# Kernel optimization log

Hardware: AMD Instinct MI355X
Metric: run time of the kernel (lower is better)

The kernel has to match this reference:

```python
import jax, jax.numpy as jnp
import numpy as np

H = 2048
MAX_DEPTH = 2
BASIS = 4


def setup_inputs() -> dict:
    key = jax.random.key(0)
    ks = jax.random.split(key, 16)
    s = 0.02

    def w(k, shape):
        return jax.random.normal(k, shape, dtype=jnp.float32) * s

    return dict(
        x=jax.random.normal(ks[0], (1, H), dtype=jnp.float32),
        h=jax.random.normal(ks[1], (1, H), dtype=jnp.float32),
        c=jax.random.normal(ks[2], (1, H), dtype=jnp.float32),
        Wq=w(ks[3], (H, H)), Wk=w(ks[4], (H, H)), Wv=w(ks[5], (H, H)), Wo=w(ks[6], (H, H)),
        Wih=w(ks[7], (H, 4 * H)), Whh=w(ks[8], (H, 4 * H)),
        b_lstm=jnp.zeros((4 * H,), jnp.float32),
        router_w=w(ks[9], (H, BASIS)), router_b=jnp.zeros((BASIS,), jnp.float32),
        expert_w=w(ks[10], (BASIS, H, H)), expert_b=jnp.zeros((BASIS, H), jnp.float32),
        dr_w=w(ks[11], (H, MAX_DEPTH + 1)),
        # bias the depth router toward the deepest choice so the recursion tree is exercised
        dr_b=jnp.array([0.0, 1.0, 5.0], jnp.float32),
        ram_w=w(ks[12], (2 * H, H)), ram_b=jnp.zeros((H,), jnp.float32),
        ag_w=w(ks[13], (2 * H, H)), ag_b=jnp.zeros((H,), jnp.float32),
    )


def reference(x, h, c, Wq, Wk, Wv, Wo, Wih, Whh, b_lstm, router_w, router_b,
              expert_w, expert_b, dr_w, dr_b, ram_w, ram_b, ag_w, ag_b):
    def cell_step(x_, h_, c_):
        # Single-token multi-head attention: softmax over a length-1 axis is
        # identically 1, so attention collapses to (h @ Wv) @ Wo; Wq/Wk are
        # parameters with zero effective gradient (matches torch behavior).
        attn = (h_ @ Wv) @ Wo
        gates = x_ @ Wih + attn @ Whh + b_lstm  # [1, 4H]
        i, f, g, o = jnp.split(gates, 4, axis=1)
        c2 = jax.nn.sigmoid(f) * c_ + jax.nn.sigmoid(i) * jnp.tanh(g)
        h2 = jax.nn.sigmoid(o) * jnp.tanh(c2)
        return h2, h2, c2

    def path_gate(hh):
        p = jax.nn.softmax(hh @ router_w + router_b, axis=1)          # [1, E]
        eo = jnp.einsum('bh,ehk->bek', hh, expert_w) + expert_b        # [1, E, H]
        return jnp.einsum('be,bek->bk', p, eo)                         # [1, H]

    def ramanujan(states):
        # alternating-harmonic (Ramanujan-summation style) weighted reduction
        agg = states[0] * 0.0
        for n, s in enumerate(states):
            agg = agg + (((-1.0) ** n) / (n + 1)) * s
        return jnp.concatenate([agg, states[0]], axis=1) @ ram_w + ram_b

    def fwd(x_, h_, c_, depth):
        so, hs, cs = cell_step(x_, h_, c_)
        hp = path_gate(hs)
        # mirrors torch.no_grad() + .item() host sync
        chosen = int(jnp.argmax(hp @ dr_w + dr_b, axis=1)[0])
        steps = min(chosen, max(0, MAX_DEPTH - depth))
        if steps <= 0:
            return so, hp, cs
        h_cur, c_cur, final = hp, cs, so
        states = [h_cur]
        for _ in range(steps):
            damping = 1.0 / (depth + 1) ** 2
            ro, hnr, cn = fwd(x_, h_cur, c_cur, depth + 1)
            h_next = h_cur + damping * (hnr - h_cur)  # torch.lerp
            states.append(h_next)
            h_cur, c_cur, final = h_next, cn, ro
        anchor = ramanujan(states)
        g = jax.nn.sigmoid(jnp.concatenate([h_cur, anchor], axis=1) @ ag_w + ag_b)
        return final, g * anchor + (1.0 - g) * h_cur, c_cur

    return fwd(x, h, c, 0)
```

## Files before the change

### kernel.cpp

```cpp
#include <hip/hip_runtime.h>
#include <math.h>


#define H 2048

#define DL0 0
#define DL1 4
#define DL3 8
#define GT  16
#define NODE_BASE (16 + 8192)
#define NODESZ 26624
#define O_THV   0
#define O_ATTN  2048
#define O_GATES 4096
#define O_EO    12288
#define O_SO    20480
#define O_CS    22528
#define O_HP    24576
#define FIN_BASE (NODE_BASE + 5 * NODESZ)
#define FINSZ 8192
#define O_HN     0
#define O_AGG    2048
#define O_ANCHOR 4096
#define O_GACC   6144
#define RH1 (FIN_BASE + 3 * FINSZ)
#define RF1 (RH1 + 2048)
#define RC1 (RH1 + 4096)

__device__ __forceinline__ float sigm(float v) { return 1.f / (1.f + expf(-v)); }

__device__ __forceinline__ int dsteps(const float* dl, int maxSteps) {
  float l0 = dl[0], l1 = dl[1], l2 = dl[2];
  int ch = 0; float bv = l0;
  if (l1 > bv) { bv = l1; ch = 1; }
  if (l2 > bv) { bv = l2; ch = 2; }
  return ch < maxSteps ? ch : maxSteps;
}

__device__ __forceinline__ bool pred_ok(const float* dlA, int maxA, int needA,
                                        const float* dlB, int maxB, int needB) {
  if (dlA && dsteps(dlA, maxA) < needA) return false;
  if (dlB && dsteps(dlB, maxB) < needB) return false;
  return true;
}

__global__ void k_init(float* ws, const float* b_lstm, const float* expert_b,
                       const float* ram_b, const float* ag_b, const float* dr_b) {
  const int gtid = blockIdx.x * 256 + threadIdx.x;
  const int gsz = gridDim.x * 256;
  if (gtid < 3) { ws[DL0 + gtid] = dr_b[gtid]; ws[DL1 + gtid] = dr_b[gtid]; ws[DL3 + gtid] = dr_b[gtid]; }
  for (int i = gtid; i < 8192; i += gsz) ws[GT + i] = b_lstm[i];
  for (int n = 0; n < 5; ++n) {
    float* nb = ws + NODE_BASE + n * NODESZ;
    for (int i = gtid; i < 4096; i += gsz) nb[O_THV + i] = 0.f;
    for (int i = gtid; i < 8192; i += gsz) nb[O_EO + i] = expert_b[i];
  }
  for (int f = 0; f < 3; ++f) {
    float* fb = ws + FIN_BASE + f * FINSZ;
    for (int i = gtid; i < 2048; i += gsz) { fb[O_ANCHOR + i] = ram_b[i]; fb[O_GACC + i] = ag_b[i]; }
  }
}

__global__ void k_gemv(const float* __restrict__ xA, const float* __restrict__ xB, int splitPt,
                       const float* __restrict__ W, float* __restrict__ y,
                       int K, int N, int KS,
                       const float* dlA, int maxA, int needA,
                       const float* dlB, int maxB, int needB,
                       const float* copySrc, float* copyDst, int copyN)
{
  if (!pred_ok(dlA, maxA, needA, dlB, maxB, needB)) return;
  const int tid = threadIdx.x, lane = tid & 63, tsub = tid >> 6;
  if (copySrc) {
    int gid = blockIdx.x * 256 + tid;
    if (gid < copyN) copyDst[gid] = copySrc[gid];
  }
  const int G = N >> 8;
  const int g = blockIdx.x % G;
  const int s = blockIdx.x / G;
  const int chunk = K / KS, len = chunk >> 2;
  const int i0 = s * chunk + tsub * len;
  const int j = (g << 8) + (lane << 2);
  const float* Wp = W + (size_t)i0 * N + j;
  float ax = 0.f, ay = 0.f, az = 0.f, aw = 0.f;
  for (int t = 0; t < len; ++t) {
    const int i = i0 + t;
    const float xi = (i < splitPt) ? xA[i] : xB[i - splitPt];
    const float4 wv = *reinterpret_cast<const float4*>(Wp);
    ax = fmaf(xi, wv.x, ax); ay = fmaf(xi, wv.y, ay);
    az = fmaf(xi, wv.z, az); aw = fmaf(xi, wv.w, aw);
    Wp += N;
  }
  __shared__ float4 red[256];
  red[tid] = make_float4(ax, ay, az, aw);
  __syncthreads();
  if (tsub == 0) {
    float4 a = red[tid], b = red[tid + 64], c = red[tid + 128], d = red[tid + 192];
    atomicAdd(&y[j + 0], a.x + b.x + c.x + d.x);
    atomicAdd(&y[j + 1], a.y + b.y + c.y + d.y);
    atomicAdd(&y[j + 2], a.z + b.z + c.z + d.z);
    atomicAdd(&y[j + 3], a.w + b.w + c.w + d.w);
  }
}

__global__ void k_expert(const float* __restrict__ gates, const float* __restrict__ c_in,
                         const float* __restrict__ Wex, float* __restrict__ eo,
                         float* so, float* cs,
                         const float* dlA, int maxA, int needA,
                         const float* dlB, int maxB, int needB)
{
  if (!pred_ok(dlA, maxA, needA, dlB, maxB, needB)) return;
  const int tid = threadIdx.x, lane = tid & 63, w = tid >> 6;
  const int g = blockIdx.x & 31, s = blockIdx.x >> 5;
  const int i0 = s * 128;
  __shared__ float h2s[128];
  if (tid < 128) {
    const int i = i0 + tid;
    const float gi = gates[i], gf = gates[H + i], gg = gates[2 * H + i], go = gates[3 * H + i];
    const float c2 = sigm(gf) * c_in[i] + sigm(gi) * tanhf(gg);
    const float h2 = sigm(go) * tanhf(c2);
    h2s[tid] = h2;
    if (g == 0) { so[i] = h2; cs[i] = c2; }
  }
  __syncthreads();
  const int j = (g << 8) + (lane << 2);
  const int e = j >> 11, k = j & (H - 1);
  const float* Wp = Wex + ((size_t)e << 22) + (size_t)(i0 + w * 32) * H + k;
  float ax = 0.f, ay = 0.f, az = 0.f, aw = 0.f;
  for (int t = 0; t < 32; ++t) {
    const float xi = h2s[w * 32 + t];
    const float4 wv = *reinterpret_cast<const float4*>(Wp);
    ax = fmaf(xi, wv.x, ax); ay = fmaf(xi, wv.y, ay);
    az = fmaf(xi, wv.z, az); aw = fmaf(xi, wv.w, aw);
    Wp += H;
  }
  __shared__ float4 red[256];
  red[tid] = make_float4(ax, ay, az, aw);
  __syncthreads();
  if (w == 0) {
    float4 a = red[tid], b = red[tid + 64], c = red[tid + 128], d = red[tid + 192];
    atomicAdd(&eo[j + 0], a.x + b.x + c.x + d.x);
    atomicAdd(&eo[j + 1], a.y + b.y + c.y + d.y);
    atomicAdd(&eo[j + 2], a.z + b.z + c.z + d.z);
    atomicAdd(&eo[j + 3], a.w + b.w + c.w + d.w);
  }
}

template <int LEAF>
__global__ void k_combine(const float* __restrict__ h2,
                          const float* __restrict__ router_w, const float* __restrict__ router_b,
                          const float* __restrict__ eo,
                          float* hp_out, float* dl, const float* __restrict__ dr_w,
                          const float* php, float damping, float* hn_out, float* agg_out,
                          const float* dlA, int maxA, int needA,
                          const float* dlB, int maxB, int needB)
{
  if (!pred_ok(dlA, maxA, needA, dlB, maxB, needB)) return;
  const int tid = threadIdx.x;
  float r0 = 0.f, r1 = 0.f, r2 = 0.f, r3 = 0.f;
  for (int i = tid; i < H; i += 256) {
    const float hh = h2[i];
    const float4 rw = *reinterpret_cast<const float4*>(router_w + i * 4);
    r0 = fmaf(hh, rw.x, r0); r1 = fmaf(hh, rw.y, r1);
    r2 = fmaf(hh, rw.z, r2); r3 = fmaf(hh, rw.w, r3);
  }
  __shared__ float4 red[256];
  red[tid] = make_float4(r0, r1, r2, r3);
  __syncthreads();
  for (int off = 128; off > 0; off >>= 1) {
    if (tid < off) {
      float4 b = red[tid + off];
      red[tid].x += b.x; red[tid].y += b.y; red[tid].z += b.z; red[tid].w += b.w;
    }
    __syncthreads();
  }
  const float4 L = red[0];
  __syncthreads();
  const float l0 = L.x + router_b[0], l1 = L.y + router_b[1];
  const float l2 = L.z + router_b[2], l3 = L.w + router_b[3];
  const float m = fmaxf(fmaxf(l0, l1), fmaxf(l2, l3));
  const float e0 = expf(l0 - m), e1 = expf(l1 - m), e2 = expf(l2 - m), e3 = expf(l3 - m);
  const float inv = 1.f / (e0 + e1 + e2 + e3);
  const float p0 = e0 * inv, p1 = e1 * inv, p2 = e2 * inv, p3 = e3 * inv;
  const int jj = blockIdx.x * 256 + tid;
  const float v = p0 * eo[jj] + p1 * eo[H + jj] + p2 * eo[2 * H + jj] + p3 * eo[3 * H + jj];
  if (LEAF) {
    const float h0 = php[jj];
    const float hn = h0 + damping * (v - h0);
    hn_out[jj] = hn;
    agg_out[jj] = h0 - 0.5f * hn;
  } else {
    hp_out[jj] = v;
    const float d0 = v * dr_w[jj * 3 + 0];
    const float d1 = v * dr_w[jj * 3 + 1];
    const float d2 = v * dr_w[jj * 3 + 2];
    red[tid] = make_float4(d0, d1, d2, 0.f);
    __syncthreads();
    for (int off = 128; off > 0; off >>= 1) {
      if (tid < off) {
        float4 b = red[tid + off];
        red[tid].x += b.x; red[tid].y += b.y; red[tid].z += b.z;
      }
      __syncthreads();
    }
    if (tid == 0) {
      atomicAdd(&dl[0], red[0].x);
      atomicAdd(&dl[1], red[0].y);
      atomicAdd(&dl[2], red[0].z);
    }
  }
}

__global__ void k_fsel(const float* dlC, int maxC,
                       const float* gacc, const float* anchor, const float* hn,
                       const float* soL, const float* csL,
                       const float* hpN, const float* soN, const float* csN,
                       float* rh, float* rf, float* rc,
                       const float* dlA, int maxA, int needA)
{
  if (dlA && dsteps(dlA, maxA) < needA) return;
  const int jj = blockIdx.x * 256 + threadIdx.x;
  if (dsteps(dlC, maxC) >= 1) {
    const float gv = sigm(gacc[jj]);
    rh[jj] = gv * anchor[jj] + (1.f - gv) * hn[jj];
    rf[jj] = soL[jj]; rc[jj] = csL[jj];
  } else {
    rh[jj] = hpN[jj]; rf[jj] = soN[jj]; rc[jj] = csN[jj];
  }
}

__global__ void k_tail1(const float* dl0p, const float* dl3p,
                        const float* rh1, const float* rf1, const float* rc1,
                        const float* gacc3, const float* anchor3, const float* hn3,
                        const float* so4, const float* cs4,
                        const float* hp3, const float* so3, const float* cs3,
                        const float* hp0,
                        float* agg0, float* hcur0, float* outF, float* outC)
{
  const int s0v = dsteps(dl0p, 2);
  if (s0v < 1) return;
  const int jj = blockIdx.x * 256 + threadIdx.x;
  float rh3 = 0.f, rf3 = 0.f, rc3 = 0.f;
  if (s0v >= 2) {
    if (dsteps(dl3p, 1) >= 1) {
      const float gv = sigm(gacc3[jj]);
      rh3 = gv * anchor3[jj] + (1.f - gv) * hn3[jj];
      rf3 = so4[jj]; rc3 = cs4[jj];
    } else { rh3 = hp3[jj]; rf3 = so3[jj]; rc3 = cs3[jj]; }
  }
  const float r1 = rh1[jj];
  float ag = hp0[jj] - 0.5f * r1;
  float hc, oF, oC;
  if (s0v >= 2) { ag += (1.f / 3.f) * rh3; hc = rh3; oF = rf3; oC = rc3; }
  else { hc = r1; oF = rf1[jj]; oC = rc1[jj]; }
  agg0[jj] = ag; hcur0[jj] = hc; outF[jj] = oF; outC[jj] = oC;
}

__global__ void k_tail2(const float* dl0p,
                        const float* so0, const float* hp0, const float* cs0,
                        const float* gacc0, const float* anchor0, const float* hcur0,
                        float* out)
{
  const int s0v = dsteps(dl0p, 2);
  const int jj = blockIdx.x * 256 + threadIdx.x;
  if (s0v == 0) {
    out[jj] = so0[jj]; out[H + jj] = hp0[jj]; out[2 * H + jj] = cs0[jj];
  } else {
    const float gv = sigm(gacc0[jj]);
    out[H + jj] = gv * anchor0[jj] + (1.f - gv) * hcur0[jj];
  }
}

extern "C" void kernel_launch(void* const* d_in, const int* in_sizes, int n_in,
                              void* d_out, int out_size, void* d_ws, size_t ws_size,
                              hipStream_t stream) {
  const float* x        = (const float*)d_in[0];
  const float* h0in     = (const float*)d_in[1];
  const float* c0in     = (const float*)d_in[2];
  const float* Wv       = (const float*)d_in[5];
  const float* Wo       = (const float*)d_in[6];
  const float* Wih      = (const float*)d_in[7];
  const float* Whh      = (const float*)d_in[8];
  const float* b_lstm   = (const float*)d_in[9];
  const float* router_w = (const float*)d_in[10];
  const float* router_b = (const float*)d_in[11];
  const float* expert_w = (const float*)d_in[12];
  const float* expert_b = (const float*)d_in[13];
  const float* dr_w     = (const float*)d_in[14];
  const float* dr_b     = (const float*)d_in[15];
  const float* ram_w    = (const float*)d_in[16];
  const float* ram_b    = (const float*)d_in[17];
  const float* ag_w     = (const float*)d_in[18];
  const float* ag_b     = (const float*)d_in[19];
  float* out = (float*)d_out;
  float* ws  = (float*)d_ws;

  float* dl0 = ws + DL0; float* dl1 = ws + DL1; float* dl3 = ws + DL3;
  float* gt  = ws + GT;
  auto NB = [&](int n) { return ws + NODE_BASE + n * NODESZ; };
  float* fin1 = ws + FIN_BASE;
  float* fin3 = ws + FIN_BASE + FINSZ;
  float* fin0 = ws + FIN_BASE + 2 * FINSZ;
  float* rh1 = ws + RH1; float* rf1 = ws + RF1; float* rc1 = ws + RC1;

  auto gemv = [&](const float* xA, const float* xB, int splitPt,
                  const float* W, float* y, int K, int N, int KS,
                  const float* dlA, int maxA, int needA,
                  const float* dlB, int maxB, int needB,
                  const float* cpS, float* cpD, int cpN) {
    k_gemv<<<dim3((N >> 8) * KS), dim3(256), 0, stream>>>(
        xA, xB, splitPt, W, y, K, N, KS, dlA, maxA, needA, dlB, maxB, needB, cpS, cpD, cpN);
  };

  auto node = [&](int n, const float* hv, const float* cv,
                  float* dl, float damping, const float* php, float* hn_out, float* agg_out,
                  const float* dlA, int maxA, int needA,
                  const float* dlB, int maxB, int needB) {
    float* nb = NB(n);
    float* t_hv = nb + O_THV; float* attn = nb + O_ATTN; float* gates = nb + O_GATES;
    float* eo = nb + O_EO; float* so = nb + O_SO; float* cs = nb + O_CS; float* hp = nb + O_HP;
    gemv(hv, hv, H, Wv, t_hv, H, H, 64, dlA, maxA, needA, dlB, maxB, needB, gt, gates, 4 * H);
    gemv(t_hv, t_hv, H, Wo, attn, H, H, 64, dlA, maxA, needA, dlB, maxB, needB, nullptr, nullptr, 0);
    gemv(attn, attn, H, Whh, gates, H, 4 * H, 16, dlA, maxA, needA, dlB, maxB, needB, nullptr, nullptr, 0);
    k_expert<<<dim3(512), dim3(256), 0, stream>>>(gates, cv, expert_w, eo, so, cs,
                                                  dlA, maxA, needA, dlB, maxB, needB);
    if (dl) {
      k_combine<0><<<dim3(8), dim3(256), 0, stream>>>(so, router_w, router_b, eo, hp, dl, dr_w,
                                                      nullptr, 0.f, nullptr, nullptr,
                                                      dlA, maxA, needA, dlB, maxB, needB);
    } else {
      k_combine<1><<<dim3(8), dim3(256), 0, stream>>>(so, router_w, router_b, eo, nullptr, nullptr, nullptr,
                                                      php, damping, hn_out, agg_out,
                                                      dlA, maxA, needA, dlB, maxB, needB);
    }
  };

  k_init<<<dim3(192), dim3(256), 0, stream>>>(ws, b_lstm, expert_b, ram_b, ag_b, dr_b);
  gemv(x, x, H, Wih, gt, H, 4 * H, 16, nullptr, 0, 0, nullptr, 0, 0, nullptr, nullptr, 0);

  node(0, h0in, c0in, dl0, 0.f, nullptr, nullptr, nullptr,
       nullptr, 0, 0, nullptr, 0, 0);
  node(1, NB(0) + O_HP, NB(0) + O_CS, dl1, 0.f, nullptr, nullptr, nullptr,
       dl0, 2, 1, nullptr, 0, 0);
  node(2, NB(1) + O_HP, NB(1) + O_CS, nullptr, 0.25f, NB(1) + O_HP, fin1 + O_HN, fin1 + O_AGG,
       dl0, 2, 1, dl1, 1, 1);
  gemv(fin1 + O_AGG, NB(1) + O_HP, H, ram_w, fin1 + O_ANCHOR, 2 * H, H, 64,
       dl0, 2, 1, dl1, 1, 1, nullptr, nullptr, 0);
  gemv(fin1 + O_HN, fin1 + O_ANCHOR, H, ag_w, fin1 + O_GACC, 2 * H, H, 64,
       dl0, 2, 1, dl1, 1, 1, nullptr, nullptr, 0);
  k_fsel<<<dim3(8), dim3(256), 0, stream>>>(dl1, 1,
      fin1 + O_GACC, fin1 + O_ANCHOR, fin1 + O_HN,
      NB(2) + O_SO, NB(2) + O_CS,
      NB(1) + O_HP, NB(1) + O_SO, NB(1) + O_CS,
      rh1, rf1, rc1, dl0, 2, 1);

  node(3, rh1, rc1, dl3, 0.f, nullptr, nullptr, nullptr,
       dl0, 2, 2, nullptr, 0, 0);
  node(4, NB(3) + O_HP, NB(3) + O_CS, nullptr, 0.25f, NB(3) + O_HP, fin3 + O_HN, fin3 + O_AGG,
       dl0, 2, 2, dl3, 1, 1);
  gemv(fin3 + O_AGG, NB(3) + O_HP, H, ram_w, fin3 + O_ANCHOR, 2 * H, H, 64,
       dl0, 2, 2, dl3, 1, 1, nullptr, nullptr, 0);
  gemv(fin3 + O_HN, fin3 + O_ANCHOR, H, ag_w, fin3 + O_GACC, 2 * H, H, 64,
       dl0, 2, 2, dl3, 1, 1, nullptr, nullptr, 0);

  k_tail1<<<dim3(8), dim3(256), 0, stream>>>(dl0, dl3,
      rh1, rf1, rc1,
      fin3 + O_GACC, fin3 + O_ANCHOR, fin3 + O_HN,
      NB(4) + O_SO, NB(4) + O_CS,
      NB(3) + O_HP, NB(3) + O_SO, NB(3) + O_CS,
      NB(0) + O_HP,
      fin0 + O_AGG, fin0 + O_HN, out, out + 2 * H);
  gemv(fin0 + O_AGG, NB(0) + O_HP, H, ram_w, fin0 + O_ANCHOR, 2 * H, H, 64,
       dl0, 2, 1, nullptr, 0, 0, nullptr, nullptr, 0);
  gemv(fin0 + O_HN, fin0 + O_ANCHOR, H, ag_w, fin0 + O_GACC, 2 * H, H, 64,
       dl0, 2, 1, nullptr, 0, 0, nullptr, nullptr, 0);
  k_tail2<<<dim3(8), dim3(256), 0, stream>>>(dl0,
      NB(0) + O_SO, NB(0) + O_HP, NB(0) + O_CS,
      fin0 + O_GACC, fin0 + O_ANCHOR, fin0 + O_HN, out);
}
```

Measured before the change: 406.2 us.

## Convert recurrent weights to bf16 per call and fuse combine/tail kernels via last-block counters

Each call now converts Wv, Wo, Whh and the expert weights to bf16 in a workspace region, and the per-node GEMVs and expert kernel stream those bf16 weights with 8-wide loads. Halving the bytes read over the five node passes is meant to cut the HBM traffic that dominates these GEMVs, even after paying the conversion traffic once per call. The router/combine step and the fsel/tail steps are folded into the preceding kernels using an atomic last-block counter, and fixed 256-block grids replace the per-shape launch sizes. This reduces launch count, but it costs bf16 rounding error in the recurrence and adds threadfence/atomic serialization at the end of each kernel.

```diff
diff --git a/kernel.cpp b/kernel.cpp
--- a/kernel.cpp
+++ b/kernel.cpp
@@ -3,116 +3,250 @@
 
 
 #define H 2048
-
-#define DL0 0
-#define DL1 4
-#define DL3 8
-#define GT  16
-#define NODE_BASE (16 + 8192)
-#define NODESZ 26624
-#define O_THV   0
-#define O_ATTN  2048
-#define O_GATES 4096
-#define O_EO    12288
-#define O_SO    20480
-#define O_CS    22528
-#define O_HP    24576
-#define FIN_BASE (NODE_BASE + 5 * NODESZ)
-#define FINSZ 8192
-#define O_HN     0
-#define O_AGG    2048
-#define O_ANCHOR 4096
-#define O_GACC   6144
-#define RH1 (FIN_BASE + 3 * FINSZ)
-#define RF1 (RH1 + 2048)
-#define RC1 (RH1 + 4096)
+typedef unsigned short u16;
+
+constexpr int DL_OFF   = 16;
+constexpr int GT_OFF   = 32;
+constexpr int NODE_OFF = 8224;
+constexpr int NODESZ   = 26624;
+constexpr int THVo = 0, ATTNo = 2048, GATESo = 4096, EOo = 12288, SOo = 20480, CSo = 22528, HPo = 24576;
+constexpr int FIN_OFF  = NODE_OFF + 5 * NODESZ;
+constexpr int FINSZ    = 8192;
+constexpr int HNo = 0, AGGo = 2048, ANCo = 4096, GACCo = 6144;
+constexpr int RH1_OFF  = FIN_OFF + 3 * FINSZ;
+constexpr int RF1_OFF  = RH1_OFF + 2048;
+constexpr int RC1_OFF  = RH1_OFF + 4096;
+constexpr size_t BF_BYTE_OFF = 688384;
+constexpr size_t oWv = 0;
+constexpr size_t oWo = 4194304;
+constexpr size_t oWhh = 8388608;
+constexpr size_t oEx = 25165824;
+constexpr size_t BF_CONV_ELEMS = 41943040;
 
 __device__ __forceinline__ float sigm(float v) { return 1.f / (1.f + expf(-v)); }
 
-__device__ __forceinline__ int dsteps(const float* dl, int maxSteps) {
+__device__ __forceinline__ int dsteps(const float* dl, int mx) {
   float l0 = dl[0], l1 = dl[1], l2 = dl[2];
   int ch = 0; float bv = l0;
   if (l1 > bv) { bv = l1; ch = 1; }
   if (l2 > bv) { bv = l2; ch = 2; }
-  return ch < maxSteps ? ch : maxSteps;
-}
-
-__device__ __forceinline__ bool pred_ok(const float* dlA, int maxA, int needA,
-                                        const float* dlB, int maxB, int needB) {
-  if (dlA && dsteps(dlA, maxA) < needA) return false;
-  if (dlB && dsteps(dlB, maxB) < needB) return false;
+  return ch < mx ? ch : mx;
+}
+
+__device__ __forceinline__ bool pred(const float* ws, int code) {
+  if (code == 0) return true;
+  const int s0 = dsteps(ws + DL_OFF, 2);
+  switch (code) {
+    case 1: return s0 >= 1;
+    case 2: return s0 >= 1 && dsteps(ws + DL_OFF + 4, 1) >= 1;
+    case 3: return s0 >= 2;
+    case 4: return s0 >= 2 && dsteps(ws + DL_OFF + 8, 1) >= 1;
+  }
   return true;
 }
 
-__global__ void k_init(float* ws, const float* b_lstm, const float* expert_b,
-                       const float* ram_b, const float* ag_b, const float* dr_b) {
-  const int gtid = blockIdx.x * 256 + threadIdx.x;
-  const int gsz = gridDim.x * 256;
-  if (gtid < 3) { ws[DL0 + gtid] = dr_b[gtid]; ws[DL1 + gtid] = dr_b[gtid]; ws[DL3 + gtid] = dr_b[gtid]; }
-  for (int i = gtid; i < 8192; i += gsz) ws[GT + i] = b_lstm[i];
-  for (int n = 0; n < 5; ++n) {
-    float* nb = ws + NODE_BASE + n * NODESZ;
-    for (int i = gtid; i < 4096; i += gsz) nb[O_THV + i] = 0.f;
-    for (int i = gtid; i < 8192; i += gsz) nb[O_EO + i] = expert_b[i];
-  }
-  for (int f = 0; f < 3; ++f) {
-    float* fb = ws + FIN_BASE + f * FINSZ;
-    for (int i = gtid; i < 2048; i += gsz) { fb[O_ANCHOR + i] = ram_b[i]; fb[O_GACC + i] = ag_b[i]; }
-  }
-}
-
-__global__ void k_gemv(const float* __restrict__ xA, const float* __restrict__ xB, int splitPt,
-                       const float* __restrict__ W, float* __restrict__ y,
-                       int K, int N, int KS,
-                       const float* dlA, int maxA, int needA,
-                       const float* dlB, int maxB, int needB,
-                       const float* copySrc, float* copyDst, int copyN)
+__device__ __forceinline__ float bfl(unsigned u) { union { unsigned x; float f; } c; c.x = u << 16; return c.f; }
+__device__ __forceinline__ float bfh(unsigned u) { union { unsigned x; float f; } c; c.x = u & 0xFFFF0000u; return c.f; }
+__device__ __forceinline__ u16 f2bf(float f) {
+  unsigned u = __float_as_uint(f);
+  u += 0x7FFFu + ((u >> 16) & 1u);
+  return (u16)(u >> 16);
+}
+
+template <typename WT> struct W8;
+template <> struct W8<u16> {
+  static __device__ __forceinline__ void load(const u16* p, float* w) {
+    uint4 u = *reinterpret_cast<const uint4*>(p);
+    w[0] = bfl(u.x); w[1] = bfh(u.x); w[2] = bfl(u.y); w[3] = bfh(u.y);
+    w[4] = bfl(u.z); w[5] = bfh(u.z); w[6] = bfl(u.w); w[7] = bfh(u.w);
+  }
+};
+template <> struct W8<float> {
+  static __device__ __forceinline__ void load(const float* p, float* w) {
+    float4 a = *reinterpret_cast<const float4*>(p);
+    float4 b = *reinterpret_cast<const float4*>(p + 4);
+    w[0] = a.x; w[1] = a.y; w[2] = a.z; w[3] = a.w;
+    w[4] = b.x; w[5] = b.y; w[6] = b.z; w[7] = b.w;
+  }
+};
+
+__device__ void tail_fsel(float* ws) {
+  if (dsteps(ws + DL_OFF, 2) < 1) return;
+  const bool deep = dsteps(ws + DL_OFF + 4, 1) >= 1;
+  float* rh1 = ws + RH1_OFF; float* rf1 = ws + RF1_OFF; float* rc1 = ws + RC1_OFF;
+  const float* fin = ws + FIN_OFF;
+  const float* n1 = ws + NODE_OFF + 1 * NODESZ;
+  const float* n2 = ws + NODE_OFF + 2 * NODESZ;
+  for (int jj = threadIdx.x; jj < H; jj += 256) {
+    if (deep) {
+      const float gv = sigm(fin[GACCo + jj]);
+      rh1[jj] = gv * fin[ANCo + jj] + (1.f - gv) * fin[HNo + jj];
+      rf1[jj] = n2[SOo + jj]; rc1[jj] = n2[CSo + jj];
+    } else {
+      rh1[jj] = n1[HPo + jj]; rf1[jj] = n1[SOo + jj]; rc1[jj] = n1[CSo + jj];
+    }
+  }
+}
+
+__device__ void tail1(float* ws, float* out) {
+  const int s0 = dsteps(ws + DL_OFF, 2);
+  if (s0 < 1) return;
+  const bool deep3 = dsteps(ws + DL_OFF + 8, 1) >= 1;
+  const float* rh1 = ws + RH1_OFF; const float* rf1 = ws + RF1_OFF; const float* rc1 = ws + RC1_OFF;
+  const float* fin3 = ws + FIN_OFF + FINSZ;
+  float* fin0 = ws + FIN_OFF + 2 * FINSZ;
+  const float* n3 = ws + NODE_OFF + 3 * NODESZ;
+  const float* n4 = ws + NODE_OFF + 4 * NODESZ;
+  const float* n0 = ws + NODE_OFF;
+  for (int jj = threadIdx.x; jj < H; jj += 256) {
+    float rh3 = 0.f, rf3v = 0.f, rc3v = 0.f;
+    if (s0 >= 2) {
+      if (deep3) {
+        const float gv = sigm(fin3[GACCo + jj]);
+        rh3 = gv * fin3[ANCo + jj] + (1.f - gv) * fin3[HNo + jj];
+        rf3v = n4[SOo + jj]; rc3v = n4[CSo + jj];
+      } else { rh3 = n3[HPo + jj]; rf3v = n3[SOo + jj]; rc3v = n3[CSo + jj]; }
+    }
+    const float r1 = rh1[jj];
+    float ag = n0[HPo + jj] - 0.5f * r1;
+    float hc, oF, oC;
+    if (s0 >= 2) { ag += (1.f / 3.f) * rh3; hc = rh3; oF = rf3v; oC = rc3v; }
+    else { hc = r1; oF = rf1[jj]; oC = rc1[jj]; }
+    fin0[AGGo + jj] = ag; fin0[HNo + jj] = hc;
+    out[jj] = oF; out[2 * H + jj] = oC;
+  }
+}
+
+__device__ void tail2(float* ws, float* out) {
+  const int s0 = dsteps(ws + DL_OFF, 2);
+  const float* n0 = ws + NODE_OFF;
+  const float* fin0 = ws + FIN_OFF + 2 * FINSZ;
+  for (int jj = threadIdx.x; jj < H; jj += 256) {
+    if (s0 == 0) {
+      out[jj] = n0[SOo + jj]; out[H + jj] = n0[HPo + jj]; out[2 * H + jj] = n0[CSo + jj];
+    } else {
+      const float gv = sigm(fin0[GACCo + jj]);
+      out[H + jj] = gv * fin0[ANCo + jj] + (1.f - gv) * fin0[HNo + jj];
+    }
+  }
+}
+
+__global__ void __launch_bounds__(256) k_convinit(
+    const float* Wv, const float* Wo, const float* Whh, const float* Wex,
+    const float* b_lstm, const float* expert_b, const float* ram_b, const float* ag_b,
+    float* ws, u16* bf, int doConv)
 {
-  if (!pred_ok(dlA, maxA, needA, dlB, maxB, needB)) return;
+  const int ib = (int)blockIdx.x - ((int)gridDim.x - 8);
+  if (ib >= 0) {
+    const int t = ib * 256 + threadIdx.x;
+    if (t < 16) ((unsigned*)ws)[t] = 0u;
+    for (int i = t; i < 8192; i += 2048) ws[GT_OFF + i] = b_lstm[i];
+    for (int n = 0; n < 5; ++n) {
+      float* nb = ws + NODE_OFF + n * NODESZ;
+      for (int i = t; i < 4096; i += 2048) nb[i] = 0.f;
+      for (int i = t; i < 8192; i += 2048) nb[EOo + i] = expert_b[i];
+    }
+    for (int f = 0; f < 3; ++f) {
+      float* fb = ws + FIN_OFF + f * FINSZ;
+      fb[ANCo + t] = ram_b[t];
+      fb[GACCo + t] = ag_b[t];
+    }
+    return;
+  }
+  if (!doConv) return;
+  const size_t nthr = (size_t)(gridDim.x - 8) * 256;
+  const size_t c0 = (size_t)blockIdx.x * 256 + threadIdx.x;
+  for (size_t c = c0; c < BF_CONV_ELEMS / 4; c += nthr) {
+    const size_t e = c * 4;
+    const float* src; size_t off;
+    if (e < oWo) { src = Wv; off = e; }
+    else if (e < oWhh) { src = Wo; off = e - oWo; }
+    else if (e < oEx) { src = Whh; off = e - oWhh; }
+    else { src = Wex; off = e - oEx; }
+    const float4 v = *reinterpret_cast<const float4*>(src + off);
+    ushort4 o;
+    o.x = f2bf(v.x); o.y = f2bf(v.y); o.z = f2bf(v.z); o.w = f2bf(v.w);
+    *reinterpret_cast<ushort4*>(bf + e) = o;
+  }
+}
+
+template <typename WT, int TAIL>
+__global__ void __launch_bounds__(256) k_gemv(
+    const float* __restrict__ xA, const float* __restrict__ xB, int splitPt,
+    const WT* __restrict__ W, float* __restrict__ y, int K, int N,
+    float* ws, float* out, int predCode,
+    const float* copySrc, float* copyDst, int copyN, int ctrIdx)
+{
+  const bool ok = pred(ws, predCode);
+  if (TAIL == 0 && !ok) return;
   const int tid = threadIdx.x, lane = tid & 63, tsub = tid >> 6;
-  if (copySrc) {
-    int gid = blockIdx.x * 256 + tid;
-    if (gid < copyN) copyDst[gid] = copySrc[gid];
-  }
-  const int G = N >> 8;
-  const int g = blockIdx.x % G;
-  const int s = blockIdx.x / G;
-  const int chunk = K / KS, len = chunk >> 2;
-  const int i0 = s * chunk + tsub * len;
-  const int j = (g << 8) + (lane << 2);
-  const float* Wp = W + (size_t)i0 * N + j;
-  float ax = 0.f, ay = 0.f, az = 0.f, aw = 0.f;
-  for (int t = 0; t < len; ++t) {
-    const int i = i0 + t;
-    const float xi = (i < splitPt) ? xA[i] : xB[i - splitPt];
-    const float4 wv = *reinterpret_cast<const float4*>(Wp);
-    ax = fmaf(xi, wv.x, ax); ay = fmaf(xi, wv.y, ay);
-    az = fmaf(xi, wv.z, az); aw = fmaf(xi, wv.w, aw);
-    Wp += N;
-  }
-  __shared__ float4 red[256];
-  red[tid] = make_float4(ax, ay, az, aw);
-  __syncthreads();
-  if (tsub == 0) {
-    float4 a = red[tid], b = red[tid + 64], c = red[tid + 128], d = red[tid + 192];
-    atomicAdd(&y[j + 0], a.x + b.x + c.x + d.x);
-    atomicAdd(&y[j + 1], a.y + b.y + c.y + d.y);
-    atomicAdd(&y[j + 2], a.z + b.z + c.z + d.z);
-    atomicAdd(&y[j + 3], a.w + b.w + c.w + d.w);
-  }
-}
-
-__global__ void k_expert(const float* __restrict__ gates, const float* __restrict__ c_in,
-                         const float* __restrict__ Wex, float* __restrict__ eo,
-                         float* so, float* cs,
-                         const float* dlA, int maxA, int needA,
-                         const float* dlB, int maxB, int needB)
+  __shared__ float red[2048];
+  if (ok) {
+    if (copySrc) {
+      const int gid = blockIdx.x * 256 + tid;
+      if (gid < copyN) copyDst[gid] = copySrc[gid];
+    }
+    const int G = N >> 9;
+    const int KS = gridDim.x / G;
+    const int g = blockIdx.x % G;
+    const int s = blockIdx.x / G;
+    const int chunk = K / KS, rpt = chunk >> 2;
+    const int i0 = s * chunk + tsub * rpt;
+    const int j = (g << 9) + (lane << 3);
+    const WT* Wp = W + (size_t)i0 * N + j;
+    float acc[8] = {0.f, 0.f, 0.f, 0.f, 0.f, 0.f, 0.f, 0.f};
+    for (int t = 0; t < rpt; ++t) {
+      const int i = i0 + t;
+      const float xi = (i < splitPt) ? xA[i] : xB[i - splitPt];
+      float w[8];
+      W8<WT>::load(Wp, w);
+#pragma unroll
+      for (int q = 0; q < 8; ++q) acc[q] = fmaf(xi, w[q], acc[q]);
+      Wp += N;
+    }
+#pragma unroll
+    for (int q = 0; q < 8; ++q) red[tid * 8 + q] = acc[q];
+    __syncthreads();
+    if (tsub == 0) {
+#pragma unroll
+      for (int q = 0; q < 8; ++q) {
+        const float s4 = red[tid * 8 + q] + red[(tid + 64) * 8 + q] +
+                         red[(tid + 128) * 8 + q] + red[(tid + 192) * 8 + q];
+        atomicAdd(&y[j + q], s4);
+      }
+    }
+  }
+  if (TAIL != 0) {
+    __threadfence();
+    __syncthreads();
+    __shared__ int lastF;
+    if (tid == 0) lastF = (atomicAdd((unsigned*)ws + ctrIdx, 1u) == gridDim.x - 1);
+    __syncthreads();
+    if (lastF) {
+      __threadfence();
+      if (TAIL == 1) tail_fsel(ws);
+      else if (TAIL == 2) tail1(ws, out);
+      else tail2(ws, out);
+    }
+  }
+}
+
+template <typename WT>
+__global__ void __launch_bounds__(256) k_expert(
+    const float* __restrict__ gates, const float* __restrict__ c_in,
+    const WT* __restrict__ Wex, float* ws, int predCode, int nodeIdx, int ctrIdx,
+    int dlIdx, int finIdx, float damping, int phpNodeIdx,
+    const float* __restrict__ router_w, const float* __restrict__ router_b,
+    const float* __restrict__ dr_w, const float* __restrict__ dr_b)
 {
-  if (!pred_ok(dlA, maxA, needA, dlB, maxB, needB)) return;
+  if (!pred(ws, predCode)) return;
+  float* nb = ws + NODE_OFF + nodeIdx * NODESZ;
+  float* eo = nb + EOo; float* so = nb + SOo; float* cs = nb + CSo; float* hp = nb + HPo;
   const int tid = threadIdx.x, lane = tid & 63, w = tid >> 6;
-  const int g = blockIdx.x & 31, s = blockIdx.x >> 5;
+  const int g = blockIdx.x & 15, s = blockIdx.x >> 4;
   const int i0 = s * 128;
   __shared__ float h2s[128];
+  __shared__ float red[2048];
   if (tid < 128) {
     const int i = i0 + tid;
     const float gi = gates[i], gf = gates[H + i], gg = gates[2 * H + i], go = gates[3 * H + i];
@@ -122,58 +256,54 @@
     if (g == 0) { so[i] = h2; cs[i] = c2; }
   }
   __syncthreads();
-  const int j = (g << 8) + (lane << 2);
+  const int j = (g << 9) + (lane << 3);
   const int e = j >> 11, k = j & (H - 1);
-  const float* Wp = Wex + ((size_t)e << 22) + (size_t)(i0 + w * 32) * H + k;
-  float ax = 0.f, ay = 0.f, az = 0.f, aw = 0.f;
+  const WT* Wp = Wex + ((size_t)e << 22) + (size_t)(i0 + w * 32) * H + k;
+  float acc[8] = {0.f, 0.f, 0.f, 0.f, 0.f, 0.f, 0.f, 0.f};
   for (int t = 0; t < 32; ++t) {
     const float xi = h2s[w * 32 + t];
-    const float4 wv = *reinterpret_cast<const float4*>(Wp);
-    ax = fmaf(xi, wv.x, ax); ay = fmaf(xi, wv.y, ay);
-    az = fmaf(xi, wv.z, az); aw = fmaf(xi, wv.w, aw);
+    float wv[8];
+    W8<WT>::load(Wp, wv);
+#pragma unroll
+    for (int q = 0; q < 8; ++q) acc[q] = fmaf(xi, wv[q], acc[q]);
     Wp += H;
   }
-  __shared__ float4 red[256];
-  red[tid] = make_float4(ax, ay, az, aw);
+#pragma unroll
+  for (int q = 0; q < 8; ++q) red[tid * 8 + q] = acc[q];
   __syncthreads();
   if (w == 0) {
-    float4 a = red[tid], b = red[tid + 64], c = red[tid + 128], d = red[tid + 192];
-    atomicAdd(&eo[j + 0], a.x + b.x + c.x + d.x);
-    atomicAdd(&eo[j + 1], a.y + b.y + c.y + d.y);
-    atomicAdd(&eo[j + 2], a.z + b.z + c.z + d.z);
-    atomicAdd(&eo[j + 3], a.w + b.w + c.w + d.w);
-  }
-}
-
-template <int LEAF>
-__global__ void k_combine(const float* __restrict__ h2,
-                          const float* __restrict__ router_w, const float* __restrict__ router_b,
-                          const float* __restrict__ eo,
-                          float* hp_out, float* dl, const float* __restrict__ dr_w,
-                          const float* php, float damping, float* hn_out, float* agg_out,
-                          const float* dlA, int maxA, int needA,
-                          const float* dlB, int maxB, int needB)
-{
-  if (!pred_ok(dlA, maxA, needA, dlB, maxB, needB)) return;
-  const int tid = threadIdx.x;
+#pragma unroll
+    for (int q = 0; q < 8; ++q) {
+      const float s4 = red[tid * 8 + q] + red[(tid + 64) * 8 + q] +
+                       red[(tid + 128) * 8 + q] + red[(tid + 192) * 8 + q];
+      atomicAdd(&eo[j + q], s4);
+    }
+  }
+  __threadfence();
+  __syncthreads();
+  __shared__ int lastF;
+  if (tid == 0) lastF = (atomicAdd((unsigned*)ws + ctrIdx, 1u) == gridDim.x - 1);
+  __syncthreads();
+  if (!lastF) return;
+  __threadfence();
   float r0 = 0.f, r1 = 0.f, r2 = 0.f, r3 = 0.f;
   for (int i = tid; i < H; i += 256) {
-    const float hh = h2[i];
+    const float hh = so[i];
     const float4 rw = *reinterpret_cast<const float4*>(router_w + i * 4);
     r0 = fmaf(hh, rw.x, r0); r1 = fmaf(hh, rw.y, r1);
     r2 = fmaf(hh, rw.z, r2); r3 = fmaf(hh, rw.w, r3);
   }
-  __shared__ float4 red[256];
-  red[tid] = make_float4(r0, r1, r2, r3);
+  float4* red4 = reinterpret_cast<float4*>(red);
+  red4[tid] = make_float4(r0, r1, r2, r3);
   __syncthreads();
   for (int off = 128; off > 0; off >>= 1) {
     if (tid < off) {
-      float4 b = red[tid + off];
-      red[tid].x += b.x; red[tid].y += b.y; red[tid].z += b.z; red[tid].w += b.w;
+      const float4 b = red4[tid + off];
+      red4[tid].x += b.x; red4[tid].y += b.y; red4[tid].z += b.z; red4[tid].w += b.w;
     }
     __syncthreads();
   }
-  const float4 L = red[0];
+  const float4 L = red4[0];
   __syncthreads();
   const float l0 = L.x + router_b[0], l1 = L.y + router_b[1];
   const float l2 = L.z + router_b[2], l3 = L.w + router_b[3];
@@ -181,92 +311,41 @@
   const float e0 = expf(l0 - m), e1 = expf(l1 - m), e2 = expf(l2 - m), e3 = expf(l3 - m);
   const float inv = 1.f / (e0 + e1 + e2 + e3);
   const float p0 = e0 * inv, p1 = e1 * inv, p2 = e2 * inv, p3 = e3 * inv;
-  const int jj = blockIdx.x * 256 + tid;
-  const float v = p0 * eo[jj] + p1 * eo[H + jj] + p2 * eo[2 * H + jj] + p3 * eo[3 * H + jj];
-  if (LEAF) {
-    const float h0 = php[jj];
-    const float hn = h0 + damping * (v - h0);
-    hn_out[jj] = hn;
-    agg_out[jj] = h0 - 0.5f * hn;
+  if (finIdx >= 0) {
+    const float* php = ws + NODE_OFF + phpNodeIdx * NODESZ + HPo;
+    float* hn = ws + FIN_OFF + finIdx * FINSZ + HNo;
+    float* agg = ws + FIN_OFF + finIdx * FINSZ + AGGo;
+    for (int jj = tid; jj < H; jj += 256) {
+      const float v = p0 * eo[jj] + p1 * eo[H + jj] + p2 * eo[2 * H + jj] + p3 * eo[3 * H + jj];
+      const float h0 = php[jj];
+      const float hnv = h0 + damping * (v - h0);
+      hn[jj] = hnv;
+      agg[jj] = h0 - 0.5f * hnv;
+    }
   } else {
-    hp_out[jj] = v;
-    const float d0 = v * dr_w[jj * 3 + 0];
-    const float d1 = v * dr_w[jj * 3 + 1];
-    const float d2 = v * dr_w[jj * 3 + 2];
-    red[tid] = make_float4(d0, d1, d2, 0.f);
+    float* dl = ws + DL_OFF + dlIdx * 4;
+    float d0 = 0.f, d1 = 0.f, d2 = 0.f;
+    for (int jj = tid; jj < H; jj += 256) {
+      const float v = p0 * eo[jj] + p1 * eo[H + jj] + p2 * eo[2 * H + jj] + p3 * eo[3 * H + jj];
+      hp[jj] = v;
+      d0 = fmaf(v, dr_w[jj * 3 + 0], d0);
+      d1 = fmaf(v, dr_w[jj * 3 + 1], d1);
+      d2 = fmaf(v, dr_w[jj * 3 + 2], d2);
+    }
+    red4[tid] = make_float4(d0, d1, d2, 0.f);
     __syncthreads();
     for (int off = 128; off > 0; off >>= 1) {
       if (tid < off) {
-        float4 b = red[tid + off];
-        red[tid].x += b.x; red[tid].y += b.y; red[tid].z += b.z;
+        const float4 b = red4[tid + off];
+        red4[tid].x += b.x; red4[tid].y += b.y; red4[tid].z += b.z;
       }
       __syncthreads();
     }
     if (tid == 0) {
-      atomicAdd(&dl[0], red[0].x);
-      atomicAdd(&dl[1], red[0].y);
-      atomicAdd(&dl[2], red[0].z);
-    }
-  }
-}
-
-__global__ void k_fsel(const float* dlC, int maxC,
-                       const float* gacc, const float* anchor, const float* hn,
-                       const float* soL, const float* csL,
-                       const float* hpN, const float* soN, const float* csN,
-                       float* rh, float* rf, float* rc,
-                       const float* dlA, int maxA, int needA)
-{
-  if (dlA && dsteps(dlA, maxA) < needA) return;
-  const int jj = blockIdx.x * 256 + threadIdx.x;
-  if (dsteps(dlC, maxC) >= 1) {
-    const float gv = sigm(gacc[jj]);
-    rh[jj] = gv * anchor[jj] + (1.f - gv) * hn[jj];
-    rf[jj] = soL[jj]; rc[jj] = csL[jj];
-  } else {
-    rh[jj] = hpN[jj]; rf[jj] = soN[jj]; rc[jj] = csN[jj];
-  }
-}
-
-__global__ void k_tail1(const float* dl0p, const float* dl3p,
-                        const float* rh1, const float* rf1, const float* rc1,
-                        const float* gacc3, const float* anchor3, const float* hn3,
-                        const float* so4, const float* cs4,
-                        const float* hp3, const float* so3, const float* cs3,
-                        const float* hp0,
-                        float* agg0, float* hcur0, float* outF, float* outC)
-{
-  const int s0v = dsteps(dl0p, 2);
-  if (s0v < 1) return;
-  const int jj = blockIdx.x * 256 + threadIdx.x;
-  float rh3 = 0.f, rf3 = 0.f, rc3 = 0.f;
-  if (s0v >= 2) {
-    if (dsteps(dl3p, 1) >= 1) {
-      const float gv = sigm(gacc3[jj]);
-      rh3 = gv * anchor3[jj] + (1.f - gv) * hn3[jj];
-      rf3 = so4[jj]; rc3 = cs4[jj];
-    } else { rh3 = hp3[jj]; rf3 = so3[jj]; rc3 = cs3[jj]; }
-  }
-  const float r1 = rh1[jj];
-  float ag = hp0[jj] - 0.5f * r1;
-  float hc, oF, oC;
-  if (s0v >= 2) { ag += (1.f / 3.f) * rh3; hc = rh3; oF = rf3; oC = rc3; }
-  else { hc = r1; oF = rf1[jj]; oC = rc1[jj]; }
-  agg0[jj] = ag; hcur0[jj] = hc; outF[jj] = oF; outC[jj] = oC;
-}
-
-__global__ void k_tail2(const float* dl0p,
-                        const float* so0, const float* hp0, const float* cs0,
-                        const float* gacc0, const float* anchor0, const float* hcur0,
-                        float* out)
-{
-  const int s0v = dsteps(dl0p, 2);
-  const int jj = blockIdx.x * 256 + threadIdx.x;
-  if (s0v == 0) {
-    out[jj] = so0[jj]; out[H + jj] = hp0[jj]; out[2 * H + jj] = cs0[jj];
-  } else {
-    const float gv = sigm(gacc0[jj]);
-    out[H + jj] = gv * anchor0[jj] + (1.f - gv) * hcur0[jj];
+      dl[0] = red4[0].x + dr_b[0];
+      dl[1] = red4[0].y + dr_b[1];
+      dl[2] = red4[0].z + dr_b[2];
+    }
   }
 }
 
@@ -294,86 +373,63 @@
   float* out = (float*)d_out;
   float* ws  = (float*)d_ws;
 
-  float* dl0 = ws + DL0; float* dl1 = ws + DL1; float* dl3 = ws + DL3;
-  float* gt  = ws + GT;
-  auto NB = [&](int n) { return ws + NODE_BASE + n * NODESZ; };
-  float* fin1 = ws + FIN_BASE;
-  float* fin3 = ws + FIN_BASE + FINSZ;
-  float* fin0 = ws + FIN_BASE + 2 * FINSZ;
-  float* rh1 = ws + RH1; float* rf1 = ws + RF1; float* rc1 = ws + RC1;
-
-  auto gemv = [&](const float* xA, const float* xB, int splitPt,
-                  const float* W, float* y, int K, int N, int KS,
-                  const float* dlA, int maxA, int needA,
-                  const float* dlB, int maxB, int needB,
-                  const float* cpS, float* cpD, int cpN) {
-    k_gemv<<<dim3((N >> 8) * KS), dim3(256), 0, stream>>>(
-        xA, xB, splitPt, W, y, K, N, KS, dlA, maxA, needA, dlB, maxB, needB, cpS, cpD, cpN);
+  const bool useBf = ws_size >= BF_BYTE_OFF + BF_CONV_ELEMS * 2 + 1024;
+  u16* bf = (u16*)((char*)d_ws + BF_BYTE_OFF);
+  const u16 *bWv = bf + oWv, *bWo = bf + oWo, *bWhh = bf + oWhh, *bEx = bf + oEx;
+
+  auto nbuf = [&](int n) { return ws + NODE_OFF + n * NODESZ; };
+  float* fin0 = ws + FIN_OFF;
+  float* fin1 = ws + FIN_OFF + FINSZ;
+  float* fin2 = ws + FIN_OFF + 2 * FINSZ;
+
+  auto gemvB = [&](const float* xA, const float* xB, int splitPt, const u16* Wb, const float* Wf,
+                   float* y, int K, int N, int predCode,
+                   const float* cpS, float* cpD, int cpN) {
+    if (useBf)
+      k_gemv<u16, 0><<<256, 256, 0, stream>>>(xA, xB, splitPt, Wb, y, K, N, ws, out, predCode, cpS, cpD, cpN, 0);
+    else
+      k_gemv<float, 0><<<256, 256, 0, stream>>>(xA, xB, splitPt, Wf, y, K, N, ws, out, predCode, cpS, cpD, cpN, 0);
   };
-
-  auto node = [&](int n, const float* hv, const float* cv,
-                  float* dl, float damping, const float* php, float* hn_out, float* agg_out,
-                  const float* dlA, int maxA, int needA,
-                  const float* dlB, int maxB, int needB) {
-    float* nb = NB(n);
-    float* t_hv = nb + O_THV; float* attn = nb + O_ATTN; float* gates = nb + O_GATES;
-    float* eo = nb + O_EO; float* so = nb + O_SO; float* cs = nb + O_CS; float* hp = nb + O_HP;
-    gemv(hv, hv, H, Wv, t_hv, H, H, 64, dlA, maxA, needA, dlB, maxB, needB, gt, gates, 4 * H);
-    gemv(t_hv, t_hv, H, Wo, attn, H, H, 64, dlA, maxA, needA, dlB, maxB, needB, nullptr, nullptr, 0);
-    gemv(attn, attn, H, Whh, gates, H, 4 * H, 16, dlA, maxA, needA, dlB, maxB, needB, nullptr, nullptr, 0);
-    k_expert<<<dim3(512), dim3(256), 0, stream>>>(gates, cv, expert_w, eo, so, cs,
-                                                  dlA, maxA, needA, dlB, maxB, needB);
-    if (dl) {
-      k_combine<0><<<dim3(8), dim3(256), 0, stream>>>(so, router_w, router_b, eo, hp, dl, dr_w,
-                                                      nullptr, 0.f, nullptr, nullptr,
-                                                      dlA, maxA, needA, dlB, maxB, needB);
-    } else {
-      k_combine<1><<<dim3(8), dim3(256), 0, stream>>>(so, router_w, router_b, eo, nullptr, nullptr, nullptr,
-                                                      php, damping, hn_out, agg_out,
-                                                      dlA, maxA, needA, dlB, maxB, needB);
+  auto gemvF = [&](const float* xA, const float* xB, int splitPt, const float* Wf,
+                   float* y, int K, int N, int predCode, int tail, int ctrIdx) {
+    switch (tail) {
+      case 0: k_gemv<float, 0><<<256, 256, 0, stream>>>(xA, xB, splitPt, Wf, y, K, N, ws, out, predCode, nullptr, nullptr, 0, ctrIdx); break;
+      case 1: k_gemv<float, 1><<<256, 256, 0, stream>>>(xA, xB, splitPt, Wf, y, K, N, ws, out, predCode, nullptr, nullptr, 0, ctrIdx); break;
+      case 2: k_gemv<float, 2><<<256, 256, 0, stream>>>(xA, xB, splitPt, Wf, y, K, N, ws, out, predCode, nullptr, nullptr, 0, ctrIdx); break;
+      default: k_gemv<float, 3><<<256, 256, 0, stream>>>(xA, xB, splitPt, Wf, y, K, N, ws, out, predCode, nullptr, nullptr, 0, ctrIdx); break;
     }
   };
 
-  k_init<<<dim3(192), dim3(256), 0, stream>>>(ws, b_lstm, expert_b, ram_b, ag_b, dr_b);
-  gemv(x, x, H, Wih, gt, H, 4 * H, 16, nullptr, 0, 0, nullptr, 0, 0, nullptr, nullptr, 0);
-
-  node(0, h0in, c0in, dl0, 0.f, nullptr, nullptr, nullptr,
-       nullptr, 0, 0, nullptr, 0, 0);
-  node(1, NB(0) + O_HP, NB(0) + O_CS, dl1, 0.f, nullptr, nullptr, nullptr,
-       dl0, 2, 1, nullptr, 0, 0);
-  node(2, NB(1) + O_HP, NB(1) + O_CS, nullptr, 0.25f, NB(1) + O_HP, fin1 + O_HN, fin1 + O_AGG,
-       dl0, 2, 1, dl1, 1, 1);
-  gemv(fin1 + O_AGG, NB(1) + O_HP, H, ram_w, fin1 + O_ANCHOR, 2 * H, H, 64,
-       dl0, 2, 1, dl1, 1, 1, nullptr, nullptr, 0);
-  gemv(fin1 + O_HN, fin1 + O_ANCHOR, H, ag_w, fin1 + O_GACC, 2 * H, H, 64,
-       dl0, 2, 1, dl1, 1, 1, nullptr, nullptr, 0);
-  k_fsel<<<dim3(8), dim3(256), 0, stream>>>(dl1, 1,
-      fin1 + O_GACC, fin1 + O_ANCHOR, fin1 + O_HN,
-      NB(2) + O_SO, NB(2) + O_CS,
-      NB(1) + O_HP, NB(1) + O_SO, NB(1) + O_CS,
-      rh1, rf1, rc1, dl0, 2, 1);
-
-  node(3, rh1, rc1, dl3, 0.f, nullptr, nullptr, nullptr,
-       dl0, 2, 2, nullptr, 0, 0);
-  node(4, NB(3) + O_HP, NB(3) + O_CS, nullptr, 0.25f, NB(3) + O_HP, fin3 + O_HN, fin3 + O_AGG,
-       dl0, 2, 2, dl3, 1, 1);
-  gemv(fin3 + O_AGG, NB(3) + O_HP, H, ram_w, fin3 + O_ANCHOR, 2 * H, H, 64,
-       dl0, 2, 2, dl3, 1, 1, nullptr, nullptr, 0);
-  gemv(fin3 + O_HN, fin3 + O_ANCHOR, H, ag_w, fin3 + O_GACC, 2 * H, H, 64,
-       dl0, 2, 2, dl3, 1, 1, nullptr, nullptr, 0);
-
-  k_tail1<<<dim3(8), dim3(256), 0, stream>>>(dl0, dl3,
-      rh1, rf1, rc1,
-      fin3 + O_GACC, fin3 + O_ANCHOR, fin3 + O_HN,
-      NB(4) + O_SO, NB(4) + O_CS,
-      NB(3) + O_HP, NB(3) + O_SO, NB(3) + O_CS,
-      NB(0) + O_HP,
-      fin0 + O_AGG, fin0 + O_HN, out, out + 2 * H);
-  gemv(fin0 + O_AGG, NB(0) + O_HP, H, ram_w, fin0 + O_ANCHOR, 2 * H, H, 64,
-       dl0, 2, 1, nullptr, 0, 0, nullptr, nullptr, 0);
-  gemv(fin0 + O_HN, fin0 + O_ANCHOR, H, ag_w, fin0 + O_GACC, 2 * H, H, 64,
-       dl0, 2, 1, nullptr, 0, 0, nullptr, nullptr, 0);
-  k_tail2<<<dim3(8), dim3(256), 0, stream>>>(dl0,
-      NB(0) + O_SO, NB(0) + O_HP, NB(0) + O_CS,
-      fin0 + O_GACC, fin0 + O_ANCHOR, fin0 + O_HN, out);
-}
+  k_convinit<<<useBf ? 2056 : 8, 256, 0, stream>>>(Wv, Wo, Whh, expert_w,
+                                                   b_lstm, expert_b, ram_b, ag_b,
+                                                   ws, bf, useBf ? 1 : 0);
+  gemvF(x, x, H, Wih, ws + GT_OFF, H, 4 * H, 0, 0, 0);
+
+  auto node = [&](int n, const float* hv, const float* cv, int predCode, int ctrIdx,
+                  int dlIdx, int finIdx, float damping, int phpNodeIdx) {
+    float* nb = nbuf(n);
+    gemvB(hv, hv, H, bWv, Wv, nb + THVo, H, H, predCode, ws + GT_OFF, nb + GATESo, 8192);
+    gemvB(nb + THVo, nb + THVo, H, bWo, Wo, nb + ATTNo, H, H, predCode, nullptr, nullptr, 0);
+    gemvB(nb + ATTNo, nb + ATTNo, H, bWhh, Whh, nb + GATESo, H, 4 * H, predCode, nullptr, nullptr, 0);
+    if (useBf)
+      k_expert<u16><<<256, 256, 0, stream>>>(nb + GATESo, cv, bEx, ws, predCode, n, ctrIdx,
+                                             dlIdx, finIdx, damping, phpNodeIdx,
+                                             router_w, router_b, dr_w, dr_b);
+    else
+      k_expert<float><<<256, 256, 0, stream>>>(nb + GATESo, cv, expert_w, ws, predCode, n, ctrIdx,
+                                               dlIdx, finIdx, damping, phpNodeIdx,
+                                               router_w, router_b, dr_w, dr_b);
+  };
+
+  node(0, h0in, c0in, 0, 0, 0, -1, 0.f, 0);
+  node(1, nbuf(0) + HPo, nbuf(0) + CSo, 1, 1, 1, -1, 0.f, 0);
+  node(2, nbuf(1) + HPo, nbuf(1) + CSo, 2, 2, -1, 0, 0.25f, 1);
+  gemvF(fin0 + AGGo, nbuf(1) + HPo, H, ram_w, fin0 + ANCo, 2 * H, H, 2, 0, 0);
+  gemvF(fin0 + HNo, fin0 + ANCo, H, ag_w, fin0 + GACCo, 2 * H, H, 2, 1, 5);
+  node(3, ws + RH1_OFF, ws + RC1_OFF, 3, 3, 2, -1, 0.f, 0);
+  node(4, nbuf(3) + HPo, nbuf(3) + CSo, 4, 4, -1, 1, 0.25f, 3);
+  gemvF(fin1 + AGGo, nbuf(3) + HPo, H, ram_w, fin1 + ANCo, 2 * H, H, 4, 0, 0);
+  gemvF(fin1 + HNo, fin1 + ANCo, H, ag_w, fin1 + GACCo, 2 * H, H, 4, 2, 6);
+  gemvF(fin2 + AGGo, nbuf(0) + HPo, H, ram_w, fin2 + ANCo, 2 * H, H, 1, 0, 0);
+  gemvF(fin2 + HNo, fin2 + ANCo, H, ag_w, fin2 + GACCo, 2 * H, H, 1, 3, 7);
+}
```

Result: slower. 678.0 us (+66.9%).
